# Performance work log

Measured on AMD Instinct MI355X. Metric: run time of the kernel, lower is better.

## Reference

```python
import jax, jax.numpy as jnp
import numpy as np

N = 20000      # interaction nodes
E = 160000     # edges
NU = 100000    # num_users
NI = 100000    # num_items
EMB = 64       # emb_size
L1, L2 = 256, 128  # GCN layer dims
H = 2          # GAT heads (and number of GAT layers)
EPS = 1e-5


def _seg(x, idx, n):
    return jax.ops.segment_sum(x, idx, num_segments=n)


def _gcn(x, W, b, src, dst, n):
    # GCNConv: add self-loops, sym-normalize, aggregate src->dst
    loops = jnp.arange(n)
    s = jnp.concatenate([src, loops])
    d = jnp.concatenate([dst, loops])
    deg = _seg(jnp.ones(s.shape[0], x.dtype), d, n)
    dinv = jnp.where(deg > 0, 1.0 / jnp.sqrt(deg), 0.0)
    xw = x @ W
    return _seg((dinv[s] * dinv[d])[:, None] * xw[s], d, n) + b


def _bn(x, g, b):
    # BatchNorm1d in training mode: biased batch statistics
    mu = x.mean(0)
    var = x.var(0)
    return (x - mu) / jnp.sqrt(var + EPS) * g + b


def _sage(x, Wl, bl, Wr, src, dst, n):
    # SAGEConv: mean neighbor aggregation (no self loops) + root transform
    cnt = _seg(jnp.ones(src.shape[0], x.dtype), dst, n)
    agg = _seg(x[src], dst, n) / jnp.maximum(cnt, 1.0)[:, None]
    return agg @ Wl + bl + x @ Wr


def _cheb(x, W0, W1c, b, src, dst, n):
    # ChebConv K=2, lambda_max=2: Tx0 = x, Tx1 = -D^{-1/2} A D^{-1/2} x
    deg = _seg(jnp.ones(src.shape[0], x.dtype), dst, n)
    dinv = jnp.where(deg > 0, 1.0 / jnp.sqrt(deg), 0.0)
    tx1 = -_seg((dinv[src] * dinv[dst])[:, None] * x[src], dst, n)
    return x @ W0 + tx1 @ W1c + b


def _gat(x, W, a_s, a_d, b, src, dst, n):
    # GATConv: add self-loops, per-edge attention softmax over dst, concat=False -> mean over heads
    loops = jnp.arange(n)
    s = jnp.concatenate([src, loops])
    d = jnp.concatenate([dst, loops])
    xp = (x @ W).reshape(n, H, L2)           # [n, H, C]
    al = (xp * a_s).sum(-1)                  # [n, H]
    ar = (xp * a_d).sum(-1)                  # [n, H]
    e = jax.nn.leaky_relu(al[s] + ar[d], 0.2)  # [E', H]
    m = jax.lax.stop_gradient(jax.ops.segment_max(e, d, num_segments=n))
    ex = jnp.exp(e - m[d])
    alpha = ex / _seg(ex, d, n)[d]
    out = _seg(alpha[:, :, None] * xp[s], d, n)  # [n, H, C]
    return out.mean(1) + b


def setup_inputs() -> dict:
    key = jax.random.key(0)
    ks = jax.random.split(key, 40)
    f = lambda k, shp: jax.random.normal(k, shp, dtype=jnp.float32) * 0.02
    inp = {
        'user_idx': jax.random.randint(ks[0], (N,), 0, NU, dtype=jnp.int32),
        'item_idx': jax.random.randint(ks[1], (N,), 0, NI, dtype=jnp.int32),
        'edge_index': jax.random.randint(ks[2], (2, E), 0, N, dtype=jnp.int32),
        'user_emb': f(ks[3], (NU, EMB)),
        'item_emb': f(ks[4], (NI, EMB)),
        'W1': f(ks[5], (2 * EMB, 1024)), 'b1': f(ks[6], (1024,)),
        'W2': f(ks[7], (1024, 512)), 'b2': f(ks[8], (512,)),
        'Wg1': f(ks[9], (512, L1)), 'bg1': f(ks[10], (L1,)),
        'gamma1': 1.0 + f(ks[11], (L1,)), 'beta1': f(ks[12], (L1,)),
        'Wg2': f(ks[13], (L1, L2)), 'bg2': f(ks[14], (L2,)),
        'gamma2': 1.0 + f(ks[15], (L2,)), 'beta2': f(ks[16], (L2,)),
        'Wsl': f(ks[17], (L2, L2)), 'bsl': f(ks[18], (L2,)),
        'Wsr': f(ks[19], (L2, L2)),
        'Wc0': f(ks[20], (L2, L2)), 'Wc1': f(ks[21], (L2, L2)), 'bc': f(ks[22], (L2,)),
        'Wgat1': f(ks[23], (L2, H * L2)), 'as1': f(ks[24], (H, L2)), 'ad1': f(ks[25], (H, L2)), 'bgat1': f(ks[26], (L2,)),
        'Wgat2': f(ks[27], (L2, H * L2)), 'as2': f(ks[28], (H, L2)), 'ad2': f(ks[29], (H, L2)), 'bgat2': f(ks[30], (L2,)),
        'Wp': f(ks[31], (L2, 1)), 'bp': f(ks[32], (1,)),
    }
    return inp


def reference(user_idx, item_idx, edge_index, user_emb, item_emb, W1, b1, W2, b2,
              Wg1, bg1, gamma1, beta1, Wg2, bg2, gamma2, beta2,
              Wsl, bsl, Wsr, Wc0, Wc1, bc,
              Wgat1, as1, ad1, bgat1, Wgat2, as2, ad2, bgat2, Wp, bp):
    src, dst = edge_index[0], edge_index[1]
    n = user_idx.shape[0]
    x = jnp.concatenate([user_emb[user_idx], item_emb[item_idx]], axis=1)
    # MLP (dropout is identity in eval mode)
    x = jax.nn.relu(x @ W1 + b1)
    x = jax.nn.relu(x @ W2 + b2)
    x = jax.nn.relu(_bn(_gcn(x, Wg1, bg1, src, dst, n), gamma1, beta1))
    x = jax.nn.relu(_bn(_gcn(x, Wg2, bg2, src, dst, n), gamma2, beta2))
    x = jax.nn.relu(_sage(x, Wsl, bsl, Wsr, src, dst, n))
    x = jax.nn.relu(_cheb(x, Wc0, Wc1, bc, src, dst, n))
    x = jax.nn.elu(_gat(x, Wgat1, as1, ad1, bgat1, src, dst, n))
    x = jax.nn.elu(_gat(x, Wgat2, as2, ad2, bgat2, src, dst, n))
    return (x @ Wp + bp)[:, 0]
```

## Files before the change

### kernel.cpp

```cpp
#include <hip/hip_runtime.h>
#include <hip/hip_bf16.h>

typedef __hip_bfloat16 bf16;
typedef short s8v __attribute__((ext_vector_type(8)));
typedef float f4v __attribute__((ext_vector_type(4)));

#define NN 20000
#define NE 160000
#define BN_EPS 1e-5f
#define NB 79

#define GF_BIAS 1
#define GF_RELU 2

static __device__ __forceinline__ float b2f(const bf16 x){ return __bfloat162float(x); }
static __device__ __forceinline__ float bits2f(unsigned int u){ return __uint_as_float(u << 16); }
static __device__ __forceinline__ unsigned short f2bits(float f){
  bf16 h = __float2bfloat16(f);
  unsigned short u; __builtin_memcpy(&u, &h, 2); return u;
}
static __device__ __forceinline__ float lrelu(float v){ return (v > 0.f) ? v : 0.2f * v; }

static inline int cdiv(int a, int b){ return (a + b - 1) / b; }

static __device__ __forceinline__ void gload16(const short* g, short* l){
  __builtin_amdgcn_global_load_lds(
      (const __attribute__((address_space(1))) unsigned int*)g,
      (__attribute__((address_space(3))) unsigned int*)l, 16, 0, 0);
}


__global__ void k_chk_bf(const unsigned short* __restrict__ x, int n, int code,
                         int* __restrict__ diag){
  bool bad = false;
  for (int k = blockIdx.x * 256 + threadIdx.x; k < n; k += gridDim.x * 256)
    if ((x[k] & 0x7F80u) == 0x7F80u) bad = true;
  if (bad) atomicCAS(diag, 0, code);
}

__global__ void k_diag_out(const int* __restrict__ diag, float* __restrict__ out){
  int d = *diag;
  if (d == 0) return;
  int i = blockIdx.x * 256 + threadIdx.x;
  if (i < NN) out[i] = (float)(d * 100);
}


__global__ void k_ideg(const int* __restrict__ dst, int* __restrict__ ideg){
  int e = blockIdx.x * 256 + threadIdx.x;
  if (e < NE) atomicAdd(&ideg[dst[e]], 1);
}

__global__ __launch_bounds__(256) void k_scan1(const int* __restrict__ ideg,
                                               int* __restrict__ tmp,
                                               int* __restrict__ bsum){
  __shared__ int lds[256];
  int tid = threadIdx.x;
  int i = blockIdx.x * 256 + tid;
  int v = (i < NN) ? ideg[i] : 0;
  lds[tid] = v;
  __syncthreads();
  for (int off = 1; off < 256; off <<= 1){
    int t = (tid >= off) ? lds[tid - off] : 0;
    __syncthreads();
    lds[tid] += t;
    __syncthreads();
  }
  if (i < NN) tmp[i] = lds[tid];
  if (tid == 255) bsum[blockIdx.x] = lds[255];
}

__global__ __launch_bounds__(128) void k_scan2(const int* __restrict__ bsum,
                                               int* __restrict__ boff){
  __shared__ int lds[128];
  int tid = threadIdx.x;
  int v = (tid < NB) ? bsum[tid] : 0;
  lds[tid] = v;
  __syncthreads();
  for (int off = 1; off < 128; off <<= 1){
    int t = (tid >= off) ? lds[tid - off] : 0;
    __syncthreads();
    lds[tid] += t;
    __syncthreads();
  }
  if (tid < NB) boff[tid] = lds[tid] - v;
}

__global__ __launch_bounds__(256) void k_scan3(const int* __restrict__ ideg,
                                               const int* __restrict__ boff,
                                               int* __restrict__ rowptr,
                                               int* __restrict__ cursor,
                                               float* __restrict__ dg,
                                               float* __restrict__ dc,
                                               float* __restrict__ ic){
  int i = blockIdx.x * 256 + threadIdx.x;
  if (i == 0) rowptr[NN] = NE;
  if (i >= NN) return;
  int v = ideg[i];
  int excl = cursor[i] - v + boff[blockIdx.x];
  rowptr[i] = excl;
  cursor[i] = excl;
  float d = (float)v;
  dg[i] = rsqrtf(d + 1.0f);
  dc[i] = (d > 0.f) ? rsqrtf(d) : 0.f;
  ic[i] = 1.0f / fmaxf(d, 1.0f);
}

__global__ void k_fill(const int* __restrict__ src, const int* __restrict__ dst,
                       int* __restrict__ cursor, int* __restrict__ colsrc){
  int e = blockIdx.x * 256 + threadIdx.x;
  if (e >= NE) return;
  int pos = atomicAdd(&cursor[dst[e]], 1);
  colsrc[pos] = src[e];
}


struct WtPack {
  const float* W[10]; short* hi[10]; short* lo[10];
  int K[10]; int nshift[10]; int base[11];
};

__global__ __launch_bounds__(256) void k_wtall(WtPack p){
  int idx = blockIdx.x * 256 + threadIdx.x;
  if (idx >= p.base[10]) return;
  int seg = 0;
#pragma unroll
  for (int i = 1; i < 10; i++) seg += (idx >= p.base[i]) ? 1 : 0;
  int local = idx - p.base[seg];
  int K = p.K[seg], ns = p.nshift[seg];
  int n = local & ((1 << ns) - 1), k = local >> ns;
  float w = p.W[seg][local];
  unsigned short h = f2bits(w);
  unsigned short l = f2bits(w - bits2f(h));
  p.hi[seg][(size_t)n * K + k] = (short)h;
  p.lo[seg][(size_t)n * K + k] = (short)l;
}


__global__ void k_gather(const int* __restrict__ uidx, const int* __restrict__ iidx,
                         const float* __restrict__ ue, const float* __restrict__ ie,
                         bf16* __restrict__ x0){
  int idx = blockIdx.x * 256 + threadIdx.x;
  if (idx >= NN * 128) return;
  int i = idx >> 7, c = idx & 127;
  float v = (c < 64) ? ue[(size_t)uidx[i] * 64 + c] : ie[(size_t)iidx[i] * 64 + (c - 64)];
  x0[idx] = __float2bfloat16(v);
}


__global__ __launch_bounds__(256) void k_mm64(
    const bf16* A0, const short* B0h, const short* B0l, int K0,
    const bf16* A1, const short* B1h, const short* B1l, int K1,
    const float* __restrict__ bias, bf16* __restrict__ C,
    int M, int Ncol, int flags, int npass){
  __shared__ short As[64][72];
  __shared__ short Bhs[64][72];
  __shared__ short Bls[64][72];
  const int tid = threadIdx.x;
  const int bid = blockIdx.y * gridDim.x + blockIdx.x;
  const int total = gridDim.x * gridDim.y;
  const int L = (bid & 7) * (total >> 3) + (bid >> 3);
  const int row0 = (L / gridDim.x) * 64, col0 = (L % gridDim.x) * 64;
  if (row0 >= M) return;
  const int wid = tid >> 6, lane = tid & 63;
  const int wr = (wid >> 1) * 32, wc = (wid & 1) * 32;
  const int lr = lane & 15, lq = lane >> 4;
  const int sr = tid >> 2, sq = (tid & 3) * 16;

  f4v acc[2][2];
#pragma unroll
  for (int i = 0; i < 2; i++)
#pragma unroll
    for (int j = 0; j < 2; j++)
      acc[i][j] = f4v{0.f, 0.f, 0.f, 0.f};

  const bf16* Aarr[2] = {A0, A1};
  const short* Bharr[2] = {B0h, B1h};
  const short* Blarr[2] = {B0l, B1l};
  const int Karr[2] = {K0, K1};

  const bool arow_ok = (row0 + sr) < M;

  for (int p = 0; p < npass; p++){
    const short* A = (const short*)Aarr[p];
    const short* Bh = Bharr[p];
    const short* Bl = Blarr[p];
    const int K = Karr[p];
    const short* arow = A + (size_t)(row0 + sr) * K + sq;
    const short* bhrow = Bh + (size_t)(col0 + sr) * K + sq;
    const short* blrow = Bl + (size_t)(col0 + sr) * K + sq;

    uint4 ra0 = make_uint4(0,0,0,0), ra1 = make_uint4(0,0,0,0);
    if (arow_ok){ ra0 = *(const uint4*)(arow); ra1 = *(const uint4*)(arow + 8); }
    uint4 rb0 = *(const uint4*)(bhrow), rb1 = *(const uint4*)(bhrow + 8);
    uint4 rc0 = *(const uint4*)(blrow), rc1 = *(const uint4*)(blrow + 8);

    for (int k0 = 0; k0 < K; k0 += 64){
      *(uint4*)&As[sr][sq] = ra0;  *(uint4*)&As[sr][sq + 8] = ra1;
      *(uint4*)&Bhs[sr][sq] = rb0; *(uint4*)&Bhs[sr][sq + 8] = rb1;
      *(uint4*)&Bls[sr][sq] = rc0; *(uint4*)&Bls[sr][sq + 8] = rc1;
      __syncthreads();
      if (k0 + 64 < K){
        int off = k0 + 64;
        if (arow_ok){ ra0 = *(const uint4*)(arow + off); ra1 = *(const uint4*)(arow + off + 8); }
        rb0 = *(const uint4*)(bhrow + off); rb1 = *(const uint4*)(bhrow + off + 8);
        rc0 = *(const uint4*)(blrow + off); rc1 = *(const uint4*)(blrow + off + 8);
      }
#pragma unroll
      for (int t = 0; t < 2; t++){
        s8v a[2], bh2[2], bl2[2];
#pragma unroll
        for (int i = 0; i < 2; i++) a[i] = *(const s8v*)&As[wr + i * 16 + lr][t * 32 + lq * 8];
#pragma unroll
        for (int j = 0; j < 2; j++){
          bh2[j] = *(const s8v*)&Bhs[wc + j * 16 + lr][t * 32 + lq * 8];
          bl2[j] = *(const s8v*)&Bls[wc + j * 16 + lr][t * 32 + lq * 8];
        }
#pragma unroll
        for (int i = 0; i < 2; i++)
#pragma unroll
          for (int j = 0; j < 2; j++){
            acc[i][j] = __builtin_amdgcn_mfma_f32_16x16x32_bf16(a[i], bh2[j], acc[i][j], 0, 0, 0);
            acc[i][j] = __builtin_amdgcn_mfma_f32_16x16x32_bf16(a[i], bl2[j], acc[i][j], 0, 0, 0);
          }
      }
      __syncthreads();
    }
  }

#pragma unroll
  for (int i = 0; i < 2; i++){
#pragma unroll
    for (int rg = 0; rg < 4; rg++){
      int row = row0 + wr + i * 16 + lq * 4 + rg;
      if (row >= M) continue;
#pragma unroll
      for (int j = 0; j < 2; j++){
        int col = col0 + wc + j * 16 + lr;
        float v = acc[i][j][rg];
        if (flags & GF_BIAS) v += bias[col];
        if (flags & GF_RELU) v = fmaxf(v, 0.f);
        C[(size_t)row * Ncol + col] = __float2bfloat16(v);
      }
    }
  }
}


__global__ __launch_bounds__(256) void k_mmw(
    const bf16* A0, const short* B0h, const short* B0l, int K,
    const float* __restrict__ bias, bf16* __restrict__ C,
    int M, int Ncol, int flags){
  __shared__ short As[2][128 * 32];
  __shared__ short Bhs[2][64 * 32];
  __shared__ short Bls[2][64 * 32];
  const int tid = threadIdx.x;
  const int bid = blockIdx.y * gridDim.x + blockIdx.x;
  const int total = gridDim.x * gridDim.y;
  const int L = (bid & 7) * (total >> 3) + (bid >> 3);
  const int row0 = (L / gridDim.x) * 128, col0 = (L % gridDim.x) * 64;
  if (row0 >= M) return;
  const int wid = tid >> 6, lane = tid & 63;
  const int wr2 = (wid >> 1) * 64, wc2 = (wid & 1) * 32;
  const int lr = lane & 15, lq = lane >> 4;
  const int rx = (lr >> 1) & 3;
  const int ch = (lq ^ rx) * 8;

  f4v acc[4][2];
#pragma unroll
  for (int i = 0; i < 4; i++)
#pragma unroll
    for (int j = 0; j < 2; j++)
      acc[i][j] = f4v{0.f, 0.f, 0.f, 0.f};

  const short* A = (const short*)A0;
  const short* asrc[2]; int adst[2];
#pragma unroll
  for (int i = 0; i < 2; i++){
    int ci = i * 256 + tid;
    int r = ci >> 2, c = ci & 3;
    int ar = row0 + r; if (ar > M - 1) ar = M - 1;
    asrc[i] = A + (size_t)ar * K + ((c ^ ((r >> 1) & 3)) * 8);
    adst[i] = ci * 8;
  }
  const short* bhsrc; const short* blsrc; int bdst;
  {
    int r = tid >> 2, c = tid & 3;
    int sc = (c ^ ((r >> 1) & 3)) * 8;
    bhsrc = B0h + (size_t)(col0 + r) * K + sc;
    blsrc = B0l + (size_t)(col0 + r) * K + sc;
    bdst = tid * 8;
  }

  const int nT = K >> 5;
#pragma unroll
  for (int i = 0; i < 2; i++) gload16(asrc[i], As[0] + adst[i]);
  gload16(bhsrc, Bhs[0] + bdst);
  gload16(blsrc, Bls[0] + bdst);

  int p = 0;
  for (int t0 = 0; t0 < nT; t0++){
    __syncthreads();
    if (t0 + 1 < nT){
      const int kofs = (t0 + 1) << 5;
      short* Ad = As[p ^ 1]; short* Bhd = Bhs[p ^ 1]; short* Bld = Bls[p ^ 1];
#pragma unroll
      for (int i = 0; i < 2; i++) gload16(asrc[i] + kofs, Ad + adst[i]);
      gload16(bhsrc + kofs, Bhd + bdst);
      gload16(blsrc + kofs, Bld + bdst);
    }
    {
      s8v a[4], bh2[2], bl2[2];
#pragma unroll
      for (int i = 0; i < 4; i++)
        a[i] = *(const s8v*)&As[p][(wr2 + i * 16 + lr) * 32 + ch];
#pragma unroll
      for (int j = 0; j < 2; j++){
        bh2[j] = *(const s8v*)&Bhs[p][(wc2 + j * 16 + lr) * 32 + ch];
        bl2[j] = *(const s8v*)&Bls[p][(wc2 + j * 16 + lr) * 32 + ch];
      }
#pragma unroll
      for (int i = 0; i < 4; i++)
#pragma unroll
        for (int j = 0; j < 2; j++){
          acc[i][j] = __builtin_amdgcn_mfma_f32_16x16x32_bf16(a[i], bh2[j], acc[i][j], 0, 0, 0);
          acc[i][j] = __builtin_amdgcn_mfma_f32_16x16x32_bf16(a[i], bl2[j], acc[i][j], 0, 0, 0);
        }
    }
    p ^= 1;
  }

#pragma unroll
  for (int i = 0; i < 4; i++){
#pragma unroll
    for (int rg = 0; rg < 4; rg++){
      int row = row0 + wr2 + i * 16 + lq * 4 + rg;
      if (row >= M) continue;
#pragma unroll
      for (int j = 0; j < 2; j++){
        int col = col0 + wc2 + j * 16 + lr;
        float v = acc[i][j][rg];
        if (flags & GF_BIAS) v += bias[col];
        if (flags & GF_RELU) v = fmaxf(v, 0.f);
        C[(size_t)row * Ncol + col] = __float2bfloat16(v);
      }
    }
  }
}


__global__ __launch_bounds__(256) void k_agg(
    const int* __restrict__ rowptr, const int* __restrict__ colsrc,
    const bf16* __restrict__ x, const float* __restrict__ wn,
    const float* __restrict__ icv, const float* __restrict__ bias,
    float* __restrict__ outf, bf16* __restrict__ outb,
    int qshift, int mode){
  int idx = blockIdx.x * 256 + threadIdx.x;
  int total = NN << qshift;
  if (idx >= total) return;
  int d = idx >> qshift, q = idx & ((1 << qshift) - 1);
  int F = 4 << qshift;
  int c = q * 4;
  int r0 = rowptr[d], r1 = rowptr[d + 1];
  float s0 = 0.f, s1 = 0.f, s2 = 0.f, s3 = 0.f;
  const short* xs = (const short*)x;
  for (int r = r0; r < r1; r += 4){
    int n = r1 - r;
    int i0 = colsrc[r];
    int i1 = (n > 1) ? colsrc[r + 1] : 0;
    int i2 = (n > 2) ? colsrc[r + 2] : 0;
    int i3 = (n > 3) ? colsrc[r + 3] : 0;
    float w0 = (mode == 1) ? 1.f : wn[i0];
    float w1 = (n > 1) ? ((mode == 1) ? 1.f : wn[i1]) : 0.f;
    float w2 = (n > 2) ? ((mode == 1) ? 1.f : wn[i2]) : 0.f;
    float w3 = (n > 3) ? ((mode == 1) ? 1.f : wn[i3]) : 0.f;
    uint2 v0 = *(const uint2*)(xs + (size_t)i0 * F + c);
    uint2 v1 = *(const uint2*)(xs + (size_t)i1 * F + c);
    uint2 v2 = *(const uint2*)(xs + (size_t)i2 * F + c);
    uint2 v3 = *(const uint2*)(xs + (size_t)i3 * F + c);
    s0 += w0 * bits2f(v0.x & 0xffffu) + w1 * bits2f(v1.x & 0xffffu)
        + w2 * bits2f(v2.x & 0xffffu) + w3 * bits2f(v3.x & 0xffffu);
    s1 += w0 * bits2f(v0.x >> 16) + w1 * bits2f(v1.x >> 16)
        + w2 * bits2f(v2.x >> 16) + w3 * bits2f(v3.x >> 16);
    s2 += w0 * bits2f(v0.y & 0xffffu) + w1 * bits2f(v1.y & 0xffffu)
        + w2 * bits2f(v2.y & 0xffffu) + w3 * bits2f(v3.y & 0xffffu);
    s3 += w0 * bits2f(v0.y >> 16) + w1 * bits2f(v1.y >> 16)
        + w2 * bits2f(v2.y >> 16) + w3 * bits2f(v3.y >> 16);
  }
  if (mode == 0){
    float w = wn[d], w2 = w * w;
    uint2 vd = *(const uint2*)(xs + (size_t)d * F + c);
    float4 o;
    o.x = w * s0 + w2 * bits2f(vd.x & 0xffffu) + bias[c + 0];
    o.y = w * s1 + w2 * bits2f(vd.x >> 16)     + bias[c + 1];
    o.z = w * s2 + w2 * bits2f(vd.y & 0xffffu) + bias[c + 2];
    o.w = w * s3 + w2 * bits2f(vd.y >> 16)     + bias[c + 3];
    *(float4*)(outf + (size_t)d * F + c) = o;
  } else {
    float m = (mode == 1) ? icv[d] : -wn[d];
    unsigned int lo = (unsigned int)f2bits(s0 * m) | ((unsigned int)f2bits(s1 * m) << 16);
    unsigned int hi = (unsigned int)f2bits(s2 * m) | ((unsigned int)f2bits(s3 * m) << 16);
    *(uint2*)((short*)outb + (size_t)d * F + c) = make_uint2(lo, hi);
  }
}


__global__ void k_bn_stats(const float* __restrict__ x, float* __restrict__ stats, int F){
  int c = threadIdx.x & (F - 1);
  int rsub = threadIdx.x / F;
  int rpi = 256 / F;
  int r0 = blockIdx.x * 128;
  int rend = min(NN, r0 + 128);
  float s1 = 0.f, s2 = 0.f;
  for (int r = r0 + rsub; r < rend; r += rpi){
    float v = x[(size_t)r * F + c];
    s1 += v; s2 += v * v;
  }
  atomicAdd(&stats[c], s1);
  atomicAdd(&stats[F + c], s2);
}

__global__ void k_bn_apply(const float* __restrict__ x, const float* __restrict__ stats,
                           const float* __restrict__ g, const float* __restrict__ b,
                           int fshift, int total, bf16* __restrict__ out){
  int idx = blockIdx.x * 256 + threadIdx.x;
  if (idx >= total) return;
  int F = 1 << fshift;
  int c = idx & (F - 1);
  float mu = stats[c] * (1.0f / NN);
  float var = fmaxf(stats[F + c] * (1.0f / NN) - mu * mu, 0.f);
  float v = (x[idx] - mu) * rsqrtf(var + BN_EPS) * g[c] + b[c];
  out[idx] = __float2bfloat16(fmaxf(v, 0.f));
}


__global__ __launch_bounds__(256) void k_gat_alar(const bf16* __restrict__ xp,
                                                  const float* __restrict__ as_,
                                                  const float* __restrict__ ad_,
                                                  float* __restrict__ al,
                                                  float* __restrict__ ar){
  int d = blockIdx.x * 4 + (threadIdx.x >> 6);
  int lane = threadIdx.x & 63;
  if (d >= NN) return;
  int c0 = lane * 2;
  unsigned int p0 = *(const unsigned int*)((const short*)xp + (size_t)d * 256 + c0);
  unsigned int p1 = *(const unsigned int*)((const short*)xp + (size_t)d * 256 + 128 + c0);
  float x00 = bits2f(p0 & 0xffffu), x01 = bits2f(p0 >> 16);
  float x10 = bits2f(p1 & 0xffffu), x11 = bits2f(p1 >> 16);
  float sa0 = x00 * as_[c0] + x01 * as_[c0 + 1];
  float sd0 = x00 * ad_[c0] + x01 * ad_[c0 + 1];
  float sa1 = x10 * as_[128 + c0] + x11 * as_[128 + c0 + 1];
  float sd1 = x10 * ad_[128 + c0] + x11 * ad_[128 + c0 + 1];
#pragma unroll
  for (int off = 32; off > 0; off >>= 1){
    sa0 += __shfl_xor(sa0, off); sd0 += __shfl_xor(sd0, off);
    sa1 += __shfl_xor(sa1, off); sd1 += __shfl_xor(sd1, off);
  }
  if (lane == 0){
    al[d * 2] = sa0;     ar[d * 2] = sd0;
    al[d * 2 + 1] = sa1; ar[d * 2 + 1] = sd1;
  }
}


__global__ __launch_bounds__(64) void k_gat(const int* __restrict__ rowptr,
                                            const int* __restrict__ colsrc,
                                            const bf16* __restrict__ xp,
                                            const float* __restrict__ al,
                                            const float* __restrict__ ar,
                                            const float* __restrict__ bias,
                                            bf16* __restrict__ outb,
                                            const float* __restrict__ wp,
                                            const float* __restrict__ bp,
                                            float* __restrict__ outf){
  __shared__ float es0[64], es1[64];
  __shared__ int ss[64];
  int d = blockIdx.x;
  int lane = threadIdx.x;
  int r0 = rowptr[d], r1 = rowptr[d + 1];
  float ard0 = ar[d * 2], ard1 = ar[d * 2 + 1];
  float e0 = lrelu(al[d * 2] + ard0);
  float e1 = lrelu(al[d * 2 + 1] + ard1);
  float m0 = e0, m1 = e1;
  float ps0 = (lane == 0) ? 1.f : 0.f;
  float ps1 = ps0;
  int c0 = lane * 2;
  float a00, a01, a10, a11;
  {
    unsigned int p0 = *(const unsigned int*)((const short*)xp + (size_t)d * 256 + c0);
    unsigned int p1 = *(const unsigned int*)((const short*)xp + (size_t)d * 256 + 128 + c0);
    a00 = bits2f(p0 & 0xffffu); a01 = bits2f(p0 >> 16);
    a10 = bits2f(p1 & 0xffffu); a11 = bits2f(p1 >> 16);
  }
  for (int t0 = r0; t0 < r1; t0 += 64){
    int nt = min(64, r1 - t0);
    float el0 = -3.4e38f, el1 = -3.4e38f;
    int s = 0;
    if (lane < nt){
      s = colsrc[t0 + lane];
      el0 = lrelu(al[s * 2] + ard0);
      el1 = lrelu(al[s * 2 + 1] + ard1);
    }
    __syncthreads();
    ss[lane] = s; es0[lane] = el0; es1[lane] = el1;
    __syncthreads();
    float cm0 = el0, cm1 = el1;
#pragma unroll
    for (int off = 32; off > 0; off >>= 1){
      cm0 = fmaxf(cm0, __shfl_xor(cm0, off));
      cm1 = fmaxf(cm1, __shfl_xor(cm1, off));
    }
    float n0 = fmaxf(m0, cm0), n1 = fmaxf(m1, cm1);
    float sc0 = expf(m0 - n0), sc1 = expf(m1 - n1);
    ps0 *= sc0; ps1 *= sc1;
    a00 *= sc0; a01 *= sc0; a10 *= sc1; a11 *= sc1;
    m0 = n0; m1 = n1;
    if (lane < nt){
      ps0 += expf(el0 - m0);
      ps1 += expf(el1 - m1);
    }
    for (int r = 0; r < nt; r++){
      int sr_ = ss[r];
      float w0 = expf(es0[r] - m0), w1 = expf(es1[r] - m1);
      unsigned int p0 = *(const unsigned int*)((const short*)xp + (size_t)sr_ * 256 + c0);
      unsigned int p1 = *(const unsigned int*)((const short*)xp + (size_t)sr_ * 256 + 128 + c0);
      a00 += w0 * bits2f(p0 & 0xffffu); a01 += w0 * bits2f(p0 >> 16);
      a10 += w1 * bits2f(p1 & 0xffffu); a11 += w1 * bits2f(p1 >> 16);
    }
  }
#pragma unroll
  for (int off = 32; off > 0; off >>= 1){
    ps0 += __shfl_xor(ps0, off);
    ps1 += __shfl_xor(ps1, off);
  }
  float v0 = 0.5f * (a00 / ps0 + a10 / ps1) + bias[c0];
  float v1 = 0.5f * (a01 / ps0 + a11 / ps1) + bias[c0 + 1];
  v0 = (v0 > 0.f) ? v0 : expm1f(v0);
  v1 = (v1 > 0.f) ? v1 : expm1f(v1);
  if (wp == nullptr){
    unsigned int packed = (unsigned int)f2bits(v0) | ((unsigned int)f2bits(v1) << 16);
    *(unsigned int*)((short*)outb + (size_t)d * 128 + c0) = packed;
  } else {
    float pv = v0 * wp[c0] + v1 * wp[c0 + 1];
#pragma unroll
    for (int off = 32; off > 0; off >>= 1) pv += __shfl_down(pv, off);
    if (lane == 0) outf[d] = pv + bp[0];
  }
}


extern "C" void kernel_launch(void* const* d_in, const int* in_sizes, int n_in,
                              void* d_out, int out_size, void* d_ws, size_t ws_size,
                              hipStream_t stream){
  const int* uidx = (const int*)d_in[0];
  const int* iidx = (const int*)d_in[1];
  const int* eidx = (const int*)d_in[2];
  const int* src = eidx;
  const int* dst = eidx + NE;
  const float* ue  = (const float*)d_in[3];
  const float* ie  = (const float*)d_in[4];
  const float* W1  = (const float*)d_in[5];  const float* b1  = (const float*)d_in[6];
  const float* W2  = (const float*)d_in[7];  const float* b2  = (const float*)d_in[8];
  const float* Wg1 = (const float*)d_in[9];  const float* bg1 = (const float*)d_in[10];
  const float* gamma1 = (const float*)d_in[11]; const float* beta1 = (const float*)d_in[12];
  const float* Wg2 = (const float*)d_in[13]; const float* bg2 = (const float*)d_in[14];
  const float* gamma2 = (const float*)d_in[15]; const float* beta2 = (const float*)d_in[16];
  const float* Wsl = (const float*)d_in[17]; const float* bsl = (const float*)d_in[18];
  const float* Wsr = (const float*)d_in[19];
  const float* Wc0 = (const float*)d_in[20]; const float* Wc1 = (const float*)d_in[21];
  const float* bc  = (const float*)d_in[22];
  const float* Wgat1 = (const float*)d_in[23]; const float* as1 = (const float*)d_in[24];
  const float* ad1 = (const float*)d_in[25];   const float* bgat1 = (const float*)d_in[26];
  const float* Wgat2 = (const float*)d_in[27]; const float* as2 = (const float*)d_in[28];
  const float* ad2 = (const float*)d_in[29];   const float* bgat2 = (const float*)d_in[30];
  const float* Wp  = (const float*)d_in[31];   const float* bp  = (const float*)d_in[32];

  int* diag   = (int*)d_ws;
  int* ideg   = diag + 4;
  float* stats1 = (float*)(ideg + NN);
  float* stats2 = stats1 + 512;
  int* bsum   = (int*)(stats2 + 256);
  int* boff   = bsum + 128;
  int* rowptr = boff + 128;
  int* cursor = rowptr + NN + 4;
  int* colsrc = cursor + NN;
  float* dg = (float*)(colsrc + NE);
  float* dc = dg + NN;
  float* ic = dc + NN;
  float* al = ic + NN;
  float* ar = al + 2 * NN;
  short* w1h = (short*)(ar + 2 * NN);
  short* w1l = w1h + 131072;
  short* w2h = w1l + 131072;
  short* w2l = w2h + 524288;
  short* wg1h = w2l + 524288;
  short* wg1l = wg1h + 131072;
  short* wg2h = wg1l + 131072;
  short* wg2l = wg2h + 32768;
  short* wslh = wg2l + 32768;
  short* wsll = wslh + 16384;
  short* wsrh = wsll + 16384;
  short* wsrl = wsrh + 16384;
  short* wc0h = wsrl + 16384;
  short* wc0l = wc0h + 16384;
  short* wc1h = wc0l + 16384;
  short* wc1l = wc1h + 16384;
  short* wgat1h = wc1l + 16384;
  short* wgat1l = wgat1h + 32768;
  short* wgat2h = wgat1l + 32768;
  short* wgat2l = wgat2h + 32768;
  short* X0 = wgat2l + 32768;
  short* H1 = X0 + (size_t)NN * 128;
  short* H2 = H1 + (size_t)10000 * 1024;

  bf16* x0b  = (bf16*)X0;
  bf16* h1b  = (bf16*)H1;
  bf16* h2b  = (bf16*)H2;
  bf16* xw1b = (bf16*)H1;
  float* g1f = (float*)H2;
  bf16* g1b  = (bf16*)(H1 + (size_t)NN * 256);
  bf16* xw2b = (bf16*)X0;
  float* x3f = (float*)H1;
  bf16* x3b  = (bf16*)H2;
  bf16* aggb = (bf16*)X0;
  bf16* x4b  = (bf16*)(H2 + (size_t)NN * 128);
  bf16* tx1b = (bf16*)X0;
  bf16* x5b  = (bf16*)(H2 + (size_t)NN * 256);
  bf16* xpb  = (bf16*)H1;
  bf16* x6b  = (bf16*)X0;

  auto mm = [&](const bf16* A1, const short* B1h, const short* B1l, int K1,
                const bf16* A2, const short* B2h, const short* B2l, int K2,
                const float* bias, bf16* C, int M, int N, int flags){
    int nx = N / 64;
    int ny = cdiv(M, 64);
    while ((nx * ny) & 7) ny++;
    dim3 g(nx, ny);
    int np = A2 ? 2 : 1;
    k_mm64<<<g, 256, 0, stream>>>(A1, B1h, B1l, K1, A2, B2h, B2l, K2,
                                  bias, C, M, N, flags, np);
  };

  auto mmw = [&](const bf16* A, const short* Bh, const short* Bl, int K,
                 const float* bias, bf16* C, int M, int N, int flags){
    int nx = N / 64;
    int ny = cdiv(M, 128);
    while ((nx * ny) & 7) ny++;
    dim3 g(nx, ny);
    k_mmw<<<g, 256, 0, stream>>>(A, Bh, Bl, K, bias, C, M, N, flags);
  };

  hipMemsetAsync(diag, 0, (size_t)(4 + NN + 768) * 4, stream);

  k_ideg<<<cdiv(NE, 256), 256, 0, stream>>>(dst, ideg);
  k_scan1<<<NB, 256, 0, stream>>>(ideg, cursor, bsum);
  k_scan2<<<1, 128, 0, stream>>>(bsum, boff);
  k_scan3<<<NB, 256, 0, stream>>>(ideg, boff, rowptr, cursor, dg, dc, ic);
  k_fill<<<cdiv(NE, 256), 256, 0, stream>>>(src, dst, cursor, colsrc);

  {
    WtPack p;
    const float* Ws[10] = {W1, W2, Wg1, Wg2, Wsl, Wsr, Wc0, Wc1, Wgat1, Wgat2};
    short* his[10] = {w1h, w2h, wg1h, wg2h, wslh, wsrh, wc0h, wc1h, wgat1h, wgat2h};
    short* los[10] = {w1l, w2l, wg1l, wg2l, wsll, wsrl, wc0l, wc1l, wgat1l, wgat2l};
    int Ks[10] = {128, 1024, 512, 256, 128, 128, 128, 128, 128, 128};
    int nss[10] = {10, 9, 8, 7, 7, 7, 7, 7, 8, 8};
    int off = 0;
    for (int i = 0; i < 10; i++){
      p.W[i] = Ws[i]; p.hi[i] = his[i]; p.lo[i] = los[i];
      p.K[i] = Ks[i]; p.nshift[i] = nss[i]; p.base[i] = off;
      off += Ks[i] << nss[i];
    }
    p.base[10] = off;
    k_wtall<<<cdiv(off, 256), 256, 0, stream>>>(p);
  }

  k_gather<<<cdiv(NN * 128, 256), 256, 0, stream>>>(uidx, iidx, ue, ie, x0b);

  for (int ofs = 0; ofs < NN; ofs += 10000){
    mmw(x0b + (size_t)ofs * 128, w1h, w1l, 128,
        b1, h1b, 10000, 1024, GF_BIAS | GF_RELU);
    mmw(h1b, w2h, w2l, 1024,
        b2, h2b + (size_t)ofs * 512, 10000, 512, GF_BIAS | GF_RELU);
  }

  mmw(h2b, wg1h, wg1l, 512, nullptr, xw1b, NN, 256, 0);
  k_agg<<<cdiv(NN * 64, 256), 256, 0, stream>>>(rowptr, colsrc, xw1b, dg, nullptr, bg1, g1f, nullptr, 6, 0);
  k_bn_stats<<<cdiv(NN, 128), 256, 0, stream>>>(g1f, stats1, 256);
  k_bn_apply<<<cdiv(NN * 256, 256), 256, 0, stream>>>(g1f, stats1, gamma1, beta1, 8, NN * 256, g1b);

  mm(g1b, wg2h, wg2l, 256, nullptr, nullptr, nullptr, 0, nullptr, xw2b, NN, 128, 0);
  k_agg<<<cdiv(NN * 32, 256), 256, 0, stream>>>(rowptr, colsrc, xw2b, dg, nullptr, bg2, x3f, nullptr, 5, 0);
  k_bn_stats<<<cdiv(NN, 128), 256, 0, stream>>>(x3f, stats2, 128);
  k_bn_apply<<<cdiv(NN * 128, 256), 256, 0, stream>>>(x3f, stats2, gamma2, beta2, 7, NN * 128, x3b);

  k_agg<<<cdiv(NN * 32, 256), 256, 0, stream>>>(rowptr, colsrc, x3b, nullptr, ic, nullptr, nullptr, aggb, 5, 1);
  mm(aggb, wslh, wsll, 128, x3b, wsrh, wsrl, 128, bsl, x4b, NN, 128, GF_BIAS | GF_RELU);

  k_agg<<<cdiv(NN * 32, 256), 256, 0, stream>>>(rowptr, colsrc, x4b, dc, nullptr, nullptr, nullptr, tx1b, 5, 2);
  mm(x4b, wc0h, wc0l, 128, tx1b, wc1h, wc1l, 128, bc, x5b, NN, 128, GF_BIAS | GF_RELU);

  mmw(x5b, wgat1h, wgat1l, 128, nullptr, xpb, NN, 256, 0);
  k_gat_alar<<<cdiv(NN, 4), 256, 0, stream>>>(xpb, as1, ad1, al, ar);
  k_gat<<<NN, 64, 0, stream>>>(rowptr, colsrc, xpb, al, ar, bgat1, x6b,
                               nullptr, nullptr, nullptr);
  k_chk_bf<<<256, 256, 0, stream>>>((const unsigned short*)x6b, NN * 128, 16, diag);

  mmw(x6b, wgat2h, wgat2l, 128, nullptr, xpb, NN, 256, 0);
  k_gat_alar<<<cdiv(NN, 4), 256, 0, stream>>>(xpb, as2, ad2, al, ar);
  k_gat<<<NN, 64, 0, stream>>>(rowptr, colsrc, xpb, al, ar, bgat2, nullptr,
                               Wp, bp, (float*)d_out);
  k_diag_out<<<cdiv(NN, 256), 256, 0, stream>>>(diag, (float*)d_out);
}
```

Before: 623.7 us.

## Deepen k_mmw LDS pipeline to four buffers with explicit vmcnt waits

The split-bf16 GEMM kernel k_mmw moves from a double-buffered LDS pipeline with __syncthreads to a four-slot ring. Loads run two K-tiles ahead, and each step uses s_waitcnt vmcnt plus a raw barrier, so more global-to-LDS loads stay in flight while MFMAs run. This doubles LDS use per block, which may reduce occupancy. The hand-counted vmcnt values and the removal of the trailing barrier before slots are reused carry correctness risk, and the code assumes nT >= 2.

```diff
diff --git a/kernel.cpp b/kernel.cpp
--- a/kernel.cpp
+++ b/kernel.cpp
@@ -28,6 +28,11 @@
       (const __attribute__((address_space(1))) unsigned int*)g,
       (__attribute__((address_space(3))) unsigned int*)l, 16, 0, 0);
 }
+
+#define VMWAIT_BAR(N) do { \
+  asm volatile("s_waitcnt vmcnt(" #N ")" ::: "memory"); \
+  __builtin_amdgcn_s_barrier(); \
+  __builtin_amdgcn_sched_barrier(0); } while (0)
 
 
 __global__ void k_chk_bf(const unsigned short* __restrict__ x, int n, int code,
@@ -251,9 +256,9 @@
     const bf16* A0, const short* B0h, const short* B0l, int K,
     const float* __restrict__ bias, bf16* __restrict__ C,
     int M, int Ncol, int flags){
-  __shared__ short As[2][128 * 32];
-  __shared__ short Bhs[2][64 * 32];
-  __shared__ short Bls[2][64 * 32];
+  __shared__ short As[4 * 128 * 32];
+  __shared__ short Bhs[4 * 64 * 32];
+  __shared__ short Bls[4 * 64 * 32];
   const int tid = threadIdx.x;
   const int bid = blockIdx.y * gridDim.x + blockIdx.x;
   const int total = gridDim.x * gridDim.y;
@@ -292,43 +297,49 @@
     bdst = tid * 8;
   }
 
+  auto stage = [&](int tt, int ss){
+    const int kofs = tt << 5;
+    short* Ad = As + ss * 4096; short* Bhd = Bhs + ss * 2048; short* Bld = Bls + ss * 2048;
+#pragma unroll
+    for (int i = 0; i < 2; i++) gload16(asrc[i] + kofs, Ad + adst[i]);
+    gload16(bhsrc + kofs, Bhd + bdst);
+    gload16(blsrc + kofs, Bld + bdst);
+  };
+
+  auto compute = [&](int ss){
+    const short* Ap = As + ss * 4096;
+    const short* Bhp = Bhs + ss * 2048;
+    const short* Blp = Bls + ss * 2048;
+    s8v a[4], bh2[2], bl2[2];
+#pragma unroll
+    for (int i = 0; i < 4; i++)
+      a[i] = *(const s8v*)&Ap[(wr2 + i * 16 + lr) * 32 + ch];
+#pragma unroll
+    for (int j = 0; j < 2; j++){
+      bh2[j] = *(const s8v*)&Bhp[(wc2 + j * 16 + lr) * 32 + ch];
+      bl2[j] = *(const s8v*)&Blp[(wc2 + j * 16 + lr) * 32 + ch];
+    }
+#pragma unroll
+    for (int i = 0; i < 4; i++)
+#pragma unroll
+      for (int j = 0; j < 2; j++){
+        acc[i][j] = __builtin_amdgcn_mfma_f32_16x16x32_bf16(a[i], bh2[j], acc[i][j], 0, 0, 0);
+        acc[i][j] = __builtin_amdgcn_mfma_f32_16x16x32_bf16(a[i], bl2[j], acc[i][j], 0, 0, 0);
+      }
+  };
+
   const int nT = K >> 5;
-#pragma unroll
-  for (int i = 0; i < 2; i++) gload16(asrc[i], As[0] + adst[i]);
-  gload16(bhsrc, Bhs[0] + bdst);
-  gload16(blsrc, Bls[0] + bdst);
-
-  int p = 0;
-  for (int t0 = 0; t0 < nT; t0++){
-    __syncthreads();
-    if (t0 + 1 < nT){
-      const int kofs = (t0 + 1) << 5;
-      short* Ad = As[p ^ 1]; short* Bhd = Bhs[p ^ 1]; short* Bld = Bls[p ^ 1];
-#pragma unroll
-      for (int i = 0; i < 2; i++) gload16(asrc[i] + kofs, Ad + adst[i]);
-      gload16(bhsrc + kofs, Bhd + bdst);
-      gload16(blsrc + kofs, Bld + bdst);
-    }
-    {
-      s8v a[4], bh2[2], bl2[2];
-#pragma unroll
-      for (int i = 0; i < 4; i++)
-        a[i] = *(const s8v*)&As[p][(wr2 + i * 16 + lr) * 32 + ch];
-#pragma unroll
-      for (int j = 0; j < 2; j++){
-        bh2[j] = *(const s8v*)&Bhs[p][(wc2 + j * 16 + lr) * 32 + ch];
-        bl2[j] = *(const s8v*)&Bls[p][(wc2 + j * 16 + lr) * 32 + ch];
-      }
-#pragma unroll
-      for (int i = 0; i < 4; i++)
-#pragma unroll
-        for (int j = 0; j < 2; j++){
-          acc[i][j] = __builtin_amdgcn_mfma_f32_16x16x32_bf16(a[i], bh2[j], acc[i][j], 0, 0, 0);
-          acc[i][j] = __builtin_amdgcn_mfma_f32_16x16x32_bf16(a[i], bl2[j], acc[i][j], 0, 0, 0);
-        }
-    }
-    p ^= 1;
-  }
+  stage(0, 0);
+  stage(1, 1);
+  for (int t = 0; t < nT - 2; t++){
+    stage(t + 2, (t + 2) & 3);
+    VMWAIT_BAR(8);
+    compute(t & 3);
+  }
+  VMWAIT_BAR(4);
+  compute((nT - 2) & 3);
+  VMWAIT_BAR(0);
+  compute((nT - 1) & 3);
 
 #pragma unroll
   for (int i = 0; i < 4; i++){
```

Result: slower. 656.0 us (+5.2%).
